# Kernel tuning notes

Measured on AMD Instinct MI355X. Metric: run time of the kernel, lower is better.

Reference implementation:

```python
import jax, jax.numpy as jnp
import numpy as np

B, S, T = 4, 1024, 1024
HID, ATT, NH = 1024, 1024, 16
HD = ATT // NH  # head size 64


def setup_inputs() -> dict:
    key = jax.random.key(0)
    ks = jax.random.split(key, 12)
    sc = 1.0 / np.sqrt(HID)
    return {
        "src": jax.random.normal(ks[0], (B, S, HID), jnp.float32),
        "tgt": jax.random.normal(ks[1], (B, T, HID), jnp.float32),
        "src_mask": jax.random.randint(ks[2], (B, S), 0, 2) > 0,
        "tgt_mask": jax.random.randint(ks[3], (B, T), 0, 2) > 0,
        "qw": jax.random.normal(ks[4], (ATT, HID), jnp.float32) * sc,
        "qb": jnp.zeros((ATT,), jnp.float32),
        "kw": jax.random.normal(ks[5], (ATT, HID), jnp.float32) * sc,
        "kb": jnp.zeros((ATT,), jnp.float32),
        "vw": jax.random.normal(ks[6], (ATT, HID), jnp.float32) * sc,
        "vb": jnp.zeros((ATT,), jnp.float32),
        "ow": jax.random.normal(ks[7], (HID, ATT), jnp.float32) * (1.0 / np.sqrt(ATT)),
        "ob": jnp.zeros((HID,), jnp.float32),
    }


def _heads(x, w, b, L):
    # x:[B,L,HID] -> [B,NH,L,HD]
    return (x @ w.T + b).reshape(B, L, NH, HD).transpose(0, 2, 1, 3)


def reference(src, tgt, src_mask, tgt_mask, qw, qb, kw, kb, vw, vb, ow, ob):
    q = _heads(src, qw, qb, S)
    k = _heads(tgt, kw, kb, T)
    v_src = _heads(src, vw, vb, S)
    v_tgt = _heads(tgt, vw, vb, T)

    attn = jnp.einsum("bhsd,bhtd->bhst", q, k) / np.sqrt(HD)  # shared scores

    sm = src_mask[:, None, :, None].astype(attn.dtype)  # [B,1,S,1]
    tm = tgt_mask[:, None, None, :].astype(attn.dtype)  # [B,1,1,T]
    NEG = 100000.0
    attn_src = attn * sm - NEG * (1.0 - sm)
    attn_tgt = attn * tm - NEG * (1.0 - tm)

    p_src = jax.nn.softmax(attn_src, axis=-1)                        # [B,H,S,T]
    p_tgt = jax.nn.softmax(attn_tgt.swapaxes(-1, -2), axis=-1)       # [B,H,T,S]

    o_src = jnp.einsum("bhst,bhtd->bhsd", p_src, v_tgt)
    o_tgt = jnp.einsum("bhts,bhsd->bhtd", p_tgt, v_src)

    o_src = o_src.transpose(0, 2, 1, 3).reshape(B, S, ATT) @ ow.T + ob
    o_tgt = o_tgt.transpose(0, 2, 1, 3).reshape(B, T, ATT) @ ow.T + ob
    return (o_src, o_tgt)
```

## Files before the change

### kernel.cpp

```cpp
#include <hip/hip_runtime.h>
#include <stdint.h>

typedef _Float16 f16;
typedef _Float16 f16x8 __attribute__((ext_vector_type(8)));
typedef _Float16 f16x4 __attribute__((ext_vector_type(4)));
typedef float    f32x4 __attribute__((ext_vector_type(4)));

#define MFMA_F16(A, B, C) __builtin_amdgcn_mfma_f32_16x16x32_f16((A), (B), (C), 0, 0, 0)

__device__ __forceinline__ void gload_lds16(const void* g, void* l) {
  __builtin_amdgcn_global_load_lds((const __attribute__((address_space(1))) void*)g,
                                   (__attribute__((address_space(3))) void*)l, 16, 0, 0);
}

__global__ void cvt_f32_f16(const float* __restrict__ s0, const float* __restrict__ s1,
                            const float* __restrict__ s2, const float* __restrict__ s3,
                            const float* __restrict__ s4, const float* __restrict__ s5,
                            f16* __restrict__ d0, f16* __restrict__ d1, f16* __restrict__ d2,
                            f16* __restrict__ d3, f16* __restrict__ d4, f16* __restrict__ d5) {
  const float* sp; f16* dp; int n4;
  switch (blockIdx.y) {
    case 0:  sp = s0; dp = d0; n4 = (4096 * 1024) / 4; break;
    case 1:  sp = s1; dp = d1; n4 = (4096 * 1024) / 4; break;
    case 2:  sp = s2; dp = d2; n4 = (1024 * 1024) / 4; break;
    case 3:  sp = s3; dp = d3; n4 = (1024 * 1024) / 4; break;
    case 4:  sp = s4; dp = d4; n4 = (1024 * 1024) / 4; break;
    default: sp = s5; dp = d5; n4 = (1024 * 1024) / 4; break;
  }
  int stride = gridDim.x * blockDim.x;
  for (int i = blockIdx.x * blockDim.x + threadIdx.x; i < n4; i += stride) {
    f32x4 v = *(const f32x4*)(sp + (size_t)i * 4);
    f16x4 h;
    h[0] = (f16)v[0]; h[1] = (f16)v[1]; h[2] = (f16)v[2]; h[3] = (f16)v[3];
    *(f16x4*)(dp + (size_t)i * 4) = h;
  }
}

__device__ __forceinline__ void gemm_core_k1024(const f16* __restrict__ A, const f16* __restrict__ W,
                                                f16* lA, f16* lB, f32x4 (&acc)[4][4],
                                                int row0, int col0) {
  const int tid = threadIdx.x;
  const int lane = tid & 63;
  const int w = tid >> 6;
  const int g = lane >> 4, c = lane & 15;
  const int wr = (w >> 1) * 64, wc = (w & 1) * 64;

  int sr[2], scol[2];
#pragma unroll
  for (int p = 0; p < 2; ++p) {
    int slot = p * 256 + tid;
    int r = slot >> 2, sph = slot & 3;
    sr[p] = r;
    scol[p] = (sph ^ ((r >> 1) & 3)) * 8;
  }
  const f16* Abase = A + (size_t)row0 * 1024;
  const f16* Wbase = W + (size_t)col0 * 1024;

  auto STAGE = [&](int nb, int k0) {
#pragma unroll
    for (int p = 0; p < 2; ++p) {
      gload_lds16(Abase + (size_t)sr[p] * 1024 + k0 + scol[p],
                  lA + nb * (128 * 32) + (p * 256 + w * 64) * 8);
      gload_lds16(Wbase + (size_t)sr[p] * 1024 + k0 + scol[p],
                  lB + nb * (128 * 32) + (p * 256 + w * 64) * 8);
    }
  };

  STAGE(0, 0);

  for (int kt = 0; kt < 32; ++kt) {
    const int cur = kt & 1;
    asm volatile("s_waitcnt vmcnt(0)" ::: "memory");
    __builtin_amdgcn_s_barrier();
    __builtin_amdgcn_sched_barrier(0);
    if (kt < 31) STAGE(cur ^ 1, (kt + 1) * 32);

    const f16* cA = lA + cur * (128 * 32);
    const f16* cB = lB + cur * (128 * 32);
    f16x8 af[4], bf[4];
#pragma unroll
    for (int m = 0; m < 4; ++m) {
      int r = wr + m * 16 + c;
      af[m] = *(const f16x8*)(cA + r * 32 + (g ^ ((r >> 1) & 3)) * 8);
    }
#pragma unroll
    for (int n = 0; n < 4; ++n) {
      int r = wc + n * 16 + c;
      bf[n] = *(const f16x8*)(cB + r * 32 + (g ^ ((r >> 1) & 3)) * 8);
    }
#pragma unroll
    for (int m = 0; m < 4; ++m)
#pragma unroll
      for (int n = 0; n < 4; ++n)
        acc[m][n] = MFMA_F16(af[m], bf[n], acc[m][n]);
  }
}

__global__ __launch_bounds__(256, 2) void proj_gemm(
    const f16* __restrict__ src16, const f16* __restrict__ tgt16,
    const f16* __restrict__ qw16, const f16* __restrict__ kw16, const f16* __restrict__ vw16,
    const float* __restrict__ qb, const float* __restrict__ kb, const float* __restrict__ vb,
    f16* __restrict__ q16, f16* __restrict__ k16, f16* __restrict__ vtS, f16* __restrict__ vtT) {
  __shared__ f16 lA[2 * 128 * 32];
  __shared__ f16 lB[2 * 128 * 32];
  const int lin = blockIdx.x;
  const int xcd = lin & 7;
  const int slot = lin >> 3;
  const int z = xcd >> 1;
  const int y = (xcd & 1) * 16 + (slot >> 3);
  const int x = slot & 7;

  const f16* A = (z & 1) ? tgt16 : src16;
  const f16* W = (z == 0) ? qw16 : (z == 1) ? kw16 : vw16;
  const float* bias = (z == 0) ? qb : (z == 1) ? kb : vb;
  const int row0 = y * 128;
  const int col0 = x * 128;
  f32x4 acc[4][4] = {};
  gemm_core_k1024(A, W, lA, lB, acc, row0, col0);

  const int lane = threadIdx.x & 63;
  const int w = threadIdx.x >> 6;
  const int g = lane >> 4, c = lane & 15;
  const int wr = (w >> 1) * 64, wc = (w & 1) * 64;

  if (z < 2) {
    f16* O = (z == 0) ? q16 : k16;
#pragma unroll
    for (int n = 0; n < 4; ++n) {
      int colg = col0 + wc + n * 16 + c;
      float bv = bias[colg];
#pragma unroll
      for (int m = 0; m < 4; ++m) {
        int rb = row0 + wr + m * 16 + g * 4;
#pragma unroll
        for (int r = 0; r < 4; ++r)
          O[(size_t)(rb + r) * 1024 + colg] = (f16)(acc[m][n][r] + bv);
      }
    }
  } else {
    f16* O = (z == 2) ? vtS : vtT;
#pragma unroll
    for (int n = 0; n < 4; ++n) {
      int colg = col0 + wc + n * 16 + c;
      float bv = bias[colg];
#pragma unroll
      for (int m = 0; m < 4; ++m) {
        int row = row0 + wr + m * 16 + g * 4;
        int bb = row >> 10, t = row & 1023;
        int tl = t & 63;
        int tp = (t & ~63) + (tl & 32) + ((tl & 12) << 1) + ((tl & 16) >> 2) + (tl & 3);
        f16x4 pk;
#pragma unroll
        for (int r = 0; r < 4; ++r) pk[r] = (f16)(acc[m][n][r] + bv);
        *(f16x4*)(O + ((size_t)(bb << 10) + colg) * 1024 + tp) = pk;
      }
    }
  }
}

__global__ __launch_bounds__(256, 2) void out_gemm(
    const f16* __restrict__ opre, const f16* __restrict__ ow16,
    const float* __restrict__ ob, float* __restrict__ out) {
  __shared__ f16 lA[2 * 128 * 32];
  __shared__ f16 lB[2 * 128 * 32];
  const int lin = blockIdx.x;
  const int xcd = lin & 7;
  const int slot = lin >> 3;
  const int y = xcd * 4 + (slot >> 2);
  const int x = slot & 3;
  const int row0 = y * 256;
  (void)row0;
  const int yy = xcd * 8 + (slot >> 1);
  (void)yy;
  const int Y = (lin >> 3);
  (void)Y;
  const int slot2 = lin >> 3;
  const int y2 = xcd * 8 + (slot2 >> 2);
  const int x2 = slot2 & 3;
  const int r0 = y2 * 128;
  const int c0 = x2 * 256;
  const int slot3 = lin >> 3;
  const int y3 = xcd * 8 + (slot3 >> 3);
  const int x3 = slot3 & 7;
  (void)r0; (void)c0; (void)x2; (void)y2; (void)slot2;
  const int row_0 = y3 * 128;
  const int col_0 = x3 * 128;
  f32x4 acc[4][4] = {};
  gemm_core_k1024(opre, ow16, lA, lB, acc, row_0, col_0);
  const int lane = threadIdx.x & 63;
  const int w = threadIdx.x >> 6;
  const int g = lane >> 4, c = lane & 15;
  const int wr = (w >> 1) * 64, wc = (w & 1) * 64;
#pragma unroll
  for (int n = 0; n < 4; ++n) {
    int colg = col_0 + wc + n * 16 + c;
    float bv = ob[colg];
#pragma unroll
    for (int m = 0; m < 4; ++m) {
      int rb = row_0 + wr + m * 16 + g * 4;
#pragma unroll
      for (int r = 0; r < 4; ++r)
        out[(size_t)(rb + r) * 1024 + colg] = acc[m][n][r] + bv;
    }
  }
}

__global__ __launch_bounds__(256, 3) void attn_fwd(
    const f16* __restrict__ q16, const f16* __restrict__ k16,
    const f16* __restrict__ vtS, const f16* __restrict__ vtT,
    const int* __restrict__ smask, const int* __restrict__ tmask,
    f16* __restrict__ opre) {
  const int bid = blockIdx.x;
  const int xcd = bid & 7;
  const int idx = bid >> 3;
  const int bhp = xcd * 16 + (idx >> 3);
  const int qblk = idx & 7;
  const int pass = bhp >> 6;
  const int bh = bhp & 63;
  const int b = bh >> 4, h = bh & 15;

  const f16* Q  = pass ? k16 : q16;
  const f16* Kt = pass ? q16 : k16;
  const f16* VT = pass ? vtS : vtT;
  const int* qmask = pass ? tmask : smask;
  const int outRowOff = pass ? 4096 : 0;

  const int tid = threadIdx.x;
  const int lane = tid & 63, wv = tid >> 6;
  const int g = lane >> 4, c = lane & 15;
  const int qrow0 = qblk * 128 + wv * 32;

  __shared__ f16 lK[2][64 * 64];
  __shared__ f16 lV[2][64 * 64];

  const size_t kbase = (size_t)b * (1024 * 1024) + h * 64;
  const size_t vbase = (size_t)bh * (64 * 1024);

  const float SC2 = 0.18033688f;
  f16x8 qf[2][2];
#pragma unroll
  for (int m = 0; m < 2; ++m) {
    f16 sh = (f16)(qmask[b * 1024 + qrow0 + m * 16 + c] ? SC2 : 0.0f);
#pragma unroll
    for (int kc = 0; kc < 2; ++kc) {
      f16x8 v = *(const f16x8*)(Q + ((size_t)(b * 1024 + qrow0 + m * 16 + c)) * 1024 + h * 64 + kc * 32 + g * 8);
#pragma unroll
      for (int j = 0; j < 8; ++j) v[j] *= sh;
      qf[m][kc] = v;
    }
  }

  auto STAGE = [&](int nb, int t0) {
#pragma unroll
    for (int i = 0; i < 2; ++i) {
      int p = i * 256 + tid;
      int row = p >> 3;
      int u = (p & 7) ^ (row & 7);
      gload_lds16(Kt + kbase + (size_t)(t0 + row) * 1024 + u * 8, &lK[nb][(i * 256 + wv * 64) * 8]);
      gload_lds16(VT + vbase + (size_t)row * 1024 + t0 + u * 8, &lV[nb][(i * 256 + wv * 64) * 8]);
    }
  };

  f32x4 accO[2][4] = {};
  float lpart[2] = {0.0f, 0.0f};

  STAGE(0, 0);

  for (int tt = 0; tt < 16; ++tt) {
    asm volatile("s_waitcnt vmcnt(0)" ::: "memory");
    __builtin_amdgcn_s_barrier();
    __builtin_amdgcn_sched_barrier(0);
    if (tt < 15) STAGE((tt + 1) & 1, (tt + 1) * 64);
    const f16* curK = lK[tt & 1];
    const f16* curV = lV[tt & 1];

    f16x8 kf[4][2];
#pragma unroll
    for (int n = 0; n < 4; ++n) {
      int row = n * 16 + c;
#pragma unroll
      for (int kc = 0; kc < 2; ++kc)
        kf[n][kc] = *(const f16x8*)(curK + row * 64 + (((kc * 4 + g) ^ (row & 7)) * 8));
    }

    f16x8 vf[4][2];
#pragma unroll
    for (int nd = 0; nd < 4; ++nd) {
      int row = nd * 16 + c;
#pragma unroll
      for (int kc = 0; kc < 2; ++kc)
        vf[nd][kc] = *(const f16x8*)(curV + row * 64 + (((kc * 4 + g) ^ (row & 7)) * 8));
    }

    f32x4 sc[2][4];
#pragma unroll
    for (int m = 0; m < 2; ++m)
#pragma unroll
      for (int n = 0; n < 4; ++n) {
        f32x4 z = {0.0f, 0.0f, 0.0f, 0.0f};
        z = MFMA_F16(kf[n][0], qf[m][0], z);
        sc[m][n] = MFMA_F16(kf[n][1], qf[m][1], z);
      }

    f16x8 pa[2][2];
#pragma unroll
    for (int m = 0; m < 2; ++m) {
      float e[16];
#pragma unroll
      for (int n = 0; n < 4; ++n)
#pragma unroll
        for (int r = 0; r < 4; ++r) e[n * 4 + r] = __builtin_amdgcn_exp2f(sc[m][n][r]);
      float s8[8];
#pragma unroll
      for (int i = 0; i < 8; ++i) s8[i] = e[i] + e[i + 8];
      float s4[4];
#pragma unroll
      for (int i = 0; i < 4; ++i) s4[i] = s8[i] + s8[i + 4];
      lpart[m] += (s4[0] + s4[1]) + (s4[2] + s4[3]);
#pragma unroll
      for (int kc = 0; kc < 2; ++kc) {
        f16x8 p8;
#pragma unroll
        for (int j = 0; j < 8; ++j) p8[j] = (f16)e[8 * kc + j];
        pa[m][kc] = p8;
      }
    }

#pragma unroll
    for (int m = 0; m < 2; ++m)
#pragma unroll
      for (int nd = 0; nd < 4; ++nd) {
        accO[m][nd] = MFMA_F16(pa[m][0], vf[nd][0], accO[m][nd]);
        accO[m][nd] = MFMA_F16(pa[m][1], vf[nd][1], accO[m][nd]);
      }
  }

#pragma unroll
  for (int m = 0; m < 2; ++m) {
    float ls = lpart[m];
    ls += __shfl_xor(ls, 16);
    ls += __shfl_xor(ls, 32);
#pragma unroll
    for (int r = 0; r < 4; ++r) {
      float lr = __shfl(ls, 20 * g + r);
      float inv = 1.0f / lr;
      size_t orow = (size_t)(outRowOff + b * 1024 + qrow0 + m * 16 + 4 * g + r);
#pragma unroll
      for (int nd = 0; nd < 4; ++nd)
        opre[orow * 1024 + h * 64 + nd * 16 + c] = (f16)(accO[m][nd][r] * inv);
    }
  }
}

extern "C" void kernel_launch(void* const* d_in, const int* in_sizes, int n_in,
                              void* d_out, int out_size, void* d_ws, size_t ws_size,
                              hipStream_t stream) {
  (void)in_sizes; (void)n_in; (void)out_size; (void)ws_size;
  const float* src = (const float*)d_in[0];
  const float* tgt = (const float*)d_in[1];
  const int*   smask = (const int*)d_in[2];
  const int*   tmask = (const int*)d_in[3];
  const float* qw = (const float*)d_in[4];
  const float* qb = (const float*)d_in[5];
  const float* kw = (const float*)d_in[6];
  const float* kb = (const float*)d_in[7];
  const float* vw = (const float*)d_in[8];
  const float* vb = (const float*)d_in[9];
  const float* ow = (const float*)d_in[10];
  const float* ob = (const float*)d_in[11];
  float* out = (float*)d_out;

  f16* wsp = (f16*)d_ws;
  const size_t M4 = (size_t)4096 * 1024;
  const size_t M1 = (size_t)1024 * 1024;
  f16* src16 = wsp;
  f16* tgt16 = src16 + M4;
  f16* qw16  = tgt16 + M4;
  f16* kw16  = qw16 + M1;
  f16* vw16  = kw16 + M1;
  f16* ow16  = vw16 + M1;
  f16* q16   = ow16 + M1;
  f16* k16   = q16 + M4;
  f16* vtS   = k16 + M4;
  f16* vtT   = vtS + M4;
  f16* opre  = wsp;

  cvt_f32_f16<<<dim3(512, 6), 256, 0, stream>>>(src, tgt, qw, kw, vw, ow,
                                                src16, tgt16, qw16, kw16, vw16, ow16);
  proj_gemm<<<dim3(1024), 256, 0, stream>>>(src16, tgt16, qw16, kw16, vw16,
                                            qb, kb, vb, q16, k16, vtS, vtT);
  attn_fwd<<<dim3(1024), 256, 0, stream>>>(q16, k16, vtS, vtT, smask, tmask, opre);
  out_gemm<<<dim3(512), 256, 0, stream>>>(opre, ow16, ob, out);
}
```

Before: 135.2 us.

## Double attention query tile per block and add MFMA priority hints

Each attention block now processes 256 query rows (64 per wave) instead of 128, halving the grid to 512 blocks so every staged K/V tile in LDS is reused by twice as many rows. The per-wave score/softmax loop is restructured to compute one m-slice at a time, and V fragment loads are moved after the softmax. s_setprio hints are wrapped around the MFMA bursts in both the attention kernel and the shared GEMM core. This raises register use (occupancy bound lowered from 3 to 2) and leaves fewer blocks to fill the GPU. The out_gemm index cleanup is cosmetic.

```diff
diff --git a/kernel.cpp b/kernel.cpp
--- a/kernel.cpp
+++ b/kernel.cpp
@@ -88,11 +88,13 @@
       int r = wc + n * 16 + c;
       bf[n] = *(const f16x8*)(cB + r * 32 + (g ^ ((r >> 1) & 3)) * 8);
     }
+    __builtin_amdgcn_s_setprio(1);
 #pragma unroll
     for (int m = 0; m < 4; ++m)
 #pragma unroll
       for (int n = 0; n < 4; ++n)
         acc[m][n] = MFMA_F16(af[m], bf[n], acc[m][n]);
+    __builtin_amdgcn_s_setprio(0);
   }
 }
 
@@ -166,38 +168,23 @@
   const int lin = blockIdx.x;
   const int xcd = lin & 7;
   const int slot = lin >> 3;
-  const int y = xcd * 4 + (slot >> 2);
-  const int x = slot & 3;
-  const int row0 = y * 256;
-  (void)row0;
-  const int yy = xcd * 8 + (slot >> 1);
-  (void)yy;
-  const int Y = (lin >> 3);
-  (void)Y;
-  const int slot2 = lin >> 3;
-  const int y2 = xcd * 8 + (slot2 >> 2);
-  const int x2 = slot2 & 3;
-  const int r0 = y2 * 128;
-  const int c0 = x2 * 256;
-  const int slot3 = lin >> 3;
-  const int y3 = xcd * 8 + (slot3 >> 3);
-  const int x3 = slot3 & 7;
-  (void)r0; (void)c0; (void)x2; (void)y2; (void)slot2;
-  const int row_0 = y3 * 128;
-  const int col_0 = x3 * 128;
+  const int y = xcd * 8 + (slot >> 3);
+  const int x = slot & 7;
+  const int row0 = y * 128;
+  const int col0 = x * 128;
   f32x4 acc[4][4] = {};
-  gemm_core_k1024(opre, ow16, lA, lB, acc, row_0, col_0);
+  gemm_core_k1024(opre, ow16, lA, lB, acc, row0, col0);
   const int lane = threadIdx.x & 63;
   const int w = threadIdx.x >> 6;
   const int g = lane >> 4, c = lane & 15;
   const int wr = (w >> 1) * 64, wc = (w & 1) * 64;
 #pragma unroll
   for (int n = 0; n < 4; ++n) {
-    int colg = col_0 + wc + n * 16 + c;
+    int colg = col0 + wc + n * 16 + c;
     float bv = ob[colg];
 #pragma unroll
     for (int m = 0; m < 4; ++m) {
-      int rb = row_0 + wr + m * 16 + g * 4;
+      int rb = row0 + wr + m * 16 + g * 4;
 #pragma unroll
       for (int r = 0; r < 4; ++r)
         out[(size_t)(rb + r) * 1024 + colg] = acc[m][n][r] + bv;
@@ -205,7 +192,7 @@
   }
 }
 
-__global__ __launch_bounds__(256, 3) void attn_fwd(
+__global__ __launch_bounds__(256, 2) void attn_fwd(
     const f16* __restrict__ q16, const f16* __restrict__ k16,
     const f16* __restrict__ vtS, const f16* __restrict__ vtT,
     const int* __restrict__ smask, const int* __restrict__ tmask,
@@ -213,8 +200,8 @@
   const int bid = blockIdx.x;
   const int xcd = bid & 7;
   const int idx = bid >> 3;
-  const int bhp = xcd * 16 + (idx >> 3);
-  const int qblk = idx & 7;
+  const int bhp = xcd * 16 + (idx >> 2);
+  const int qblk = idx & 3;
   const int pass = bhp >> 6;
   const int bh = bhp & 63;
   const int b = bh >> 4, h = bh & 15;
@@ -228,7 +215,7 @@
   const int tid = threadIdx.x;
   const int lane = tid & 63, wv = tid >> 6;
   const int g = lane >> 4, c = lane & 15;
-  const int qrow0 = qblk * 128 + wv * 32;
+  const int qrow0 = qblk * 256 + wv * 64;
 
   __shared__ f16 lK[2][64 * 64];
   __shared__ f16 lV[2][64 * 64];
@@ -237,9 +224,9 @@
   const size_t vbase = (size_t)bh * (64 * 1024);
 
   const float SC2 = 0.18033688f;
-  f16x8 qf[2][2];
-#pragma unroll
-  for (int m = 0; m < 2; ++m) {
+  f16x8 qf[4][2];
+#pragma unroll
+  for (int m = 0; m < 4; ++m) {
     f16 sh = (f16)(qmask[b * 1024 + qrow0 + m * 16 + c] ? SC2 : 0.0f);
 #pragma unroll
     for (int kc = 0; kc < 2; ++kc) {
@@ -261,8 +248,8 @@
     }
   };
 
-  f32x4 accO[2][4] = {};
-  float lpart[2] = {0.0f, 0.0f};
+  f32x4 accO[4][4] = {};
+  float lpart[4] = {0.0f, 0.0f, 0.0f, 0.0f};
 
   STAGE(0, 0);
 
@@ -283,33 +270,23 @@
         kf[n][kc] = *(const f16x8*)(curK + row * 64 + (((kc * 4 + g) ^ (row & 7)) * 8));
     }
 
-    f16x8 vf[4][2];
-#pragma unroll
-    for (int nd = 0; nd < 4; ++nd) {
-      int row = nd * 16 + c;
-#pragma unroll
-      for (int kc = 0; kc < 2; ++kc)
-        vf[nd][kc] = *(const f16x8*)(curV + row * 64 + (((kc * 4 + g) ^ (row & 7)) * 8));
-    }
-
-    f32x4 sc[2][4];
-#pragma unroll
-    for (int m = 0; m < 2; ++m)
+    f16x8 pa[4][2];
+#pragma unroll
+    for (int m = 0; m < 4; ++m) {
+      f32x4 sc[4];
+      __builtin_amdgcn_s_setprio(1);
 #pragma unroll
       for (int n = 0; n < 4; ++n) {
         f32x4 z = {0.0f, 0.0f, 0.0f, 0.0f};
         z = MFMA_F16(kf[n][0], qf[m][0], z);
-        sc[m][n] = MFMA_F16(kf[n][1], qf[m][1], z);
-      }
-
-    f16x8 pa[2][2];
-#pragma unroll
-    for (int m = 0; m < 2; ++m) {
+        sc[n] = MFMA_F16(kf[n][1], qf[m][1], z);
+      }
+      __builtin_amdgcn_s_setprio(0);
       float e[16];
 #pragma unroll
       for (int n = 0; n < 4; ++n)
 #pragma unroll
-        for (int r = 0; r < 4; ++r) e[n * 4 + r] = __builtin_amdgcn_exp2f(sc[m][n][r]);
+        for (int r = 0; r < 4; ++r) e[n * 4 + r] = __builtin_amdgcn_exp2f(sc[n][r]);
       float s8[8];
 #pragma unroll
       for (int i = 0; i < 8; ++i) s8[i] = e[i] + e[i + 8];
@@ -326,17 +303,28 @@
       }
     }
 
-#pragma unroll
-    for (int m = 0; m < 2; ++m)
+    f16x8 vf[4][2];
+#pragma unroll
+    for (int nd = 0; nd < 4; ++nd) {
+      int row = nd * 16 + c;
+#pragma unroll
+      for (int kc = 0; kc < 2; ++kc)
+        vf[nd][kc] = *(const f16x8*)(curV + row * 64 + (((kc * 4 + g) ^ (row & 7)) * 8));
+    }
+
+    __builtin_amdgcn_s_setprio(1);
+#pragma unroll
+    for (int m = 0; m < 4; ++m)
 #pragma unroll
       for (int nd = 0; nd < 4; ++nd) {
         accO[m][nd] = MFMA_F16(pa[m][0], vf[nd][0], accO[m][nd]);
         accO[m][nd] = MFMA_F16(pa[m][1], vf[nd][1], accO[m][nd]);
       }
-  }
-
-#pragma unroll
-  for (int m = 0; m < 2; ++m) {
+    __builtin_amdgcn_s_setprio(0);
+  }
+
+#pragma unroll
+  for (int m = 0; m < 4; ++m) {
     float ls = lpart[m];
     ls += __shfl_xor(ls, 16);
     ls += __shfl_xor(ls, 32);
@@ -389,6 +377,6 @@
                                                 src16, tgt16, qw16, kw16, vw16, ow16);
   proj_gemm<<<dim3(1024), 256, 0, stream>>>(src16, tgt16, qw16, kw16, vw16,
                                             qb, kb, vb, q16, k16, vtS, vtT);
-  attn_fwd<<<dim3(1024), 256, 0, stream>>>(q16, k16, vtS, vtT, smask, tmask, opre);
+  attn_fwd<<<dim3(512), 256, 0, stream>>>(q16, k16, vtS, vtT, smask, tmask, opre);
   out_gemm<<<dim3(512), 256, 0, stream>>>(opre, ow16, ob, out);
 }
```

New measurement: 127.0 us. 1.07x faster.
